# Kernel optimization log

Measured on AMD Instinct MI355X. Metric: run time of the kernel, lower is better.

The kernel has to match this reference:

```python
import jax, jax.numpy as jnp
import numpy as np

INPUT_SIZE = 512
HIDDEN_SIZE = 1024
BATCH = 16384


def setup_inputs() -> dict:
    key = jax.random.key(0)
    ks = jax.random.split(key, 11)
    s_x = 1.0 / np.sqrt(INPUT_SIZE)
    s_h = 1.0 / np.sqrt(HIDDEN_SIZE)
    inp = {
        "x": jax.random.normal(ks[0], (BATCH, INPUT_SIZE), dtype=jnp.float32),
        "hidden": jax.random.normal(ks[1], (BATCH, HIDDEN_SIZE), dtype=jnp.float32),
        # Linear weights stored as (in, out) for x @ W
        "Wxr": jax.random.uniform(ks[2], (INPUT_SIZE, HIDDEN_SIZE), jnp.float32, -s_x, s_x),
        "bxr": jax.random.uniform(ks[3], (HIDDEN_SIZE,), jnp.float32, -s_x, s_x),
        "Whr": jax.random.uniform(ks[4], (HIDDEN_SIZE, HIDDEN_SIZE), jnp.float32, -s_h, s_h),
        "Wxz": jax.random.uniform(ks[5], (INPUT_SIZE, HIDDEN_SIZE), jnp.float32, -s_x, s_x),
        "bxz": jax.random.uniform(ks[6], (HIDDEN_SIZE,), jnp.float32, -s_x, s_x),
        "Whz": jax.random.uniform(ks[7], (HIDDEN_SIZE, HIDDEN_SIZE), jnp.float32, -s_h, s_h),
        "Wxh": jax.random.uniform(ks[8], (INPUT_SIZE, HIDDEN_SIZE), jnp.float32, -s_x, s_x),
        "bxh": jax.random.uniform(ks[9], (HIDDEN_SIZE,), jnp.float32, -s_x, s_x),
        "Whh": jax.random.uniform(ks[10], (HIDDEN_SIZE, HIDDEN_SIZE), jnp.float32, -s_h, s_h),
    }
    return inp


def reference(x, hidden, Wxr, bxr, Whr, Wxz, bxz, Whz, Wxh, bxh, Whh):
    # GRU cell, single timestep.
    r = jax.nn.sigmoid(x @ Wxr + bxr + hidden @ Whr)          # reset gate (B,H)
    z = jax.nn.sigmoid(x @ Wxz + bxz + hidden @ Whz)          # update gate (B,H)
    h_cand = jnp.tanh(x @ Wxh + bxh + (r * hidden) @ Whh)     # candidate (B,H)
    return z * hidden + (1.0 - z) * h_cand
```

## Files before the change

kernel.cpp:

```cpp
#include <hip/hip_runtime.h>

typedef unsigned short u16;
typedef unsigned int u32;
typedef __bf16 bf16x8 __attribute__((ext_vector_type(8)));
typedef float f32x4 __attribute__((ext_vector_type(4)));

#define B_ROWS 16384
#define K1 1536

__device__ __forceinline__ u16 f2bf(float f) {
  u32 u = __float_as_uint(f);
  u = (u + 0x7fffu + ((u >> 16) & 1u)) >> 16;
  return (u16)u;
}
__device__ __forceinline__ float bf2f(u16 b) {
  return __uint_as_float(((u32)b) << 16);
}
__device__ __forceinline__ void gload_lds16(const void* g, void* l) {
  __builtin_amdgcn_global_load_lds((const __attribute__((address_space(1))) void*)g,
                                   (__attribute__((address_space(3))) void*)l,
                                   16, 0, 0);
}

__global__ void cvt_xh(const float* __restrict__ x, const float* __restrict__ h,
                       u16* __restrict__ xh) {
  const int iv = blockIdx.x * 256 + threadIdx.x;
  const int row = iv / 384;
  const int col = (iv - row * 384) * 4;
  const float* src = (col < 512) ? x + (size_t)row * 512 + col
                                 : h + (size_t)row * 1024 + (col - 512);
  float4 v = *(const float4*)src;
  u32 a = (u32)f2bf(v.x) | ((u32)f2bf(v.y) << 16);
  u32 b = (u32)f2bf(v.z) | ((u32)f2bf(v.w) << 16);
  *(uint2*)(xh + (size_t)row * 1536 + col) = make_uint2(a, b);
}

__global__ void transpose_cvt6(const float* __restrict__ Wxr, const float* __restrict__ Whr,
                               const float* __restrict__ Wxz, const float* __restrict__ Whz,
                               const float* __restrict__ Wxh, const float* __restrict__ Whh,
                               u16* __restrict__ W1t, u16* __restrict__ W2t) {
  __shared__ float tile[32][33];
  const int z = blockIdx.z;
  const float* W;
  u16* T;
  int Ks, koff, roff;
  switch (z) {
    case 0:  W = Wxr; T = W1t; Ks = 512;  koff = 0;   roff = 0;    break;
    case 1:  W = Whr; T = W1t; Ks = 1024; koff = 512; roff = 0;    break;
    case 2:  W = Wxz; T = W1t; Ks = 512;  koff = 0;   roff = 1024; break;
    case 3:  W = Whz; T = W1t; Ks = 1024; koff = 512; roff = 1024; break;
    case 4:  W = Wxh; T = W2t; Ks = 512;  koff = 0;   roff = 0;    break;
    default: W = Whh; T = W2t; Ks = 1024; koff = 512; roff = 0;    break;
  }
  const int bx = blockIdx.x, by = blockIdx.y;
  if (by * 32 >= Ks) return;
  const int tx = threadIdx.x, ty = threadIdx.y;
#pragma unroll
  for (int r = 0; r < 32; r += 8)
    tile[ty + r][tx] = W[(size_t)(by * 32 + ty + r) * 1024 + bx * 32 + tx];
  __syncthreads();
#pragma unroll
  for (int r = 0; r < 32; r += 8)
    T[(size_t)(roff + bx * 32 + ty + r) * K1 + koff + by * 32 + tx] = f2bf(tile[tx][ty + r]);
}

struct Src {
  const u16 *A, *B;
  u32 sA, sB;
};

__device__ __forceinline__ void gemm256(const Src& S, int nt, int brow, int bcol,
                                        u16* AsU, u16* BsU, f32x4 acc[8][4]) {
  const int tid = threadIdx.x;
  const int l = tid & 63;
  const int wid = tid >> 6;
  const int wr = wid >> 2, wc = wid & 3;
  const int lr = l & 15, kq = l >> 4;
  const int swzB = (lr & 7) * 16;
  const int kswzE = ((tid & 7) ^ ((tid >> 3) & 7)) * 8;
  const int r = tid >> 3;
  char* AsB = (char*)AsU;
  char* BsB = (char*)BsU;
  const int ldsQ = wid << 10;
  const int colK0 = (kq * 16) ^ swzB;
  const int colK1 = (64 + kq * 16) ^ swzB;
  int aRow[8], bRow[4];
#pragma unroll
  for (int m = 0; m < 8; ++m) aRow[m] = (wr * 128 + m * 16 + lr) * 128;
#pragma unroll
  for (int n = 0; n < 4; ++n) bRow[n] = (wc * 64 + n * 16 + lr) * 128;

  u32 offA[4], offB[4];
#pragma unroll
  for (int q = 0; q < 4; ++q) {
    offA[q] = (u32)((brow + q * 64 + r) * S.sA + kswzE) * 2u;
    offB[q] = (u32)((bcol + q * 64 + r) * S.sB + kswzE) * 2u;
  }

#define STG_A01(q_, c_) gload_lds16((const char*)S.A + offA[q_], \
    AsB + (c_) * 32768 + (q_) * 8192 + ldsQ)
#define STG_A23(q_, c_) gload_lds16((const char*)S.A + offA[q_], \
    AsB + (c_) * 32768 + 16384 + ((q_) - 2) * 8192 + ldsQ)
#define STG_B(q_, c_)   gload_lds16((const char*)S.B + offB[q_], \
    BsB + (c_) * 32768 + ((q_) >> 1) * 16384 + ((q_) & 1) * 8192 + ldsQ)

  STG_A01(0, 0); STG_A01(1, 0);
  STG_A23(2, 0); STG_A23(3, 0);
  STG_B(0, 0); STG_B(1, 0); STG_B(2, 0); STG_B(3, 0);
  offA[0] += 128; offA[1] += 128;
  STG_A01(0, 1); STG_A01(1, 1);
  offA[0] += 128; offA[1] += 128;
  offA[2] += 128; offA[3] += 128;
  offB[0] += 128; offB[1] += 128; offB[2] += 128; offB[3] += 128;
  asm volatile("s_waitcnt vmcnt(2)" ::: "memory");
  __builtin_amdgcn_s_barrier();
  asm volatile("" ::: "memory");

  for (int t = 0; t < nt; ++t) {
    const int c = t & 1;
    const int cb = c << 15;
    bf16x8 a[4][2], b[4][2];
#pragma unroll
    for (int m = 0; m < 4; ++m) {
      a[m][0] = *(const bf16x8*)(AsB + cb + aRow[m] + colK0);
      a[m][1] = *(const bf16x8*)(AsB + cb + aRow[m] + colK1);
    }
#pragma unroll
    for (int n = 0; n < 2; ++n) {
      b[n][0] = *(const bf16x8*)(BsB + cb + bRow[n] + colK0);
      b[n][1] = *(const bf16x8*)(BsB + cb + bRow[n] + colK1);
    }
    if (t + 1 < nt) { STG_A23(2, c ^ 1); STG_A23(3, c ^ 1); }
    __builtin_amdgcn_s_barrier();
    asm volatile("s_waitcnt lgkmcnt(0)" ::: "memory");
    __builtin_amdgcn_sched_barrier(0);
    __builtin_amdgcn_s_setprio(1);
#pragma unroll
    for (int kk = 0; kk < 2; ++kk)
#pragma unroll
      for (int m = 0; m < 4; ++m)
#pragma unroll
        for (int n = 0; n < 2; ++n)
          acc[m][n] = __builtin_amdgcn_mfma_f32_16x16x32_bf16(a[m][kk], b[n][kk], acc[m][n], 0, 0, 0);
    __builtin_amdgcn_s_setprio(0);
    __builtin_amdgcn_s_barrier();
    asm volatile("" ::: "memory");
#pragma unroll
    for (int n = 2; n < 4; ++n) {
      b[n][0] = *(const bf16x8*)(BsB + cb + bRow[n] + colK0);
      b[n][1] = *(const bf16x8*)(BsB + cb + bRow[n] + colK1);
    }
    if (t + 1 < nt) { STG_B(0, c ^ 1); STG_B(1, c ^ 1); }
    __builtin_amdgcn_s_barrier();
    asm volatile("s_waitcnt lgkmcnt(0)" ::: "memory");
    __builtin_amdgcn_sched_barrier(0);
    __builtin_amdgcn_s_setprio(1);
#pragma unroll
    for (int kk = 0; kk < 2; ++kk)
#pragma unroll
      for (int m = 0; m < 4; ++m)
#pragma unroll
        for (int n = 2; n < 4; ++n)
          acc[m][n] = __builtin_amdgcn_mfma_f32_16x16x32_bf16(a[m][kk], b[n][kk], acc[m][n], 0, 0, 0);
    __builtin_amdgcn_s_setprio(0);
    __builtin_amdgcn_s_barrier();
    asm volatile("" ::: "memory");
#pragma unroll
    for (int m = 0; m < 4; ++m) {
      a[m][0] = *(const bf16x8*)(AsB + cb + aRow[m + 4] + colK0);
      a[m][1] = *(const bf16x8*)(AsB + cb + aRow[m + 4] + colK1);
    }
    if (t + 1 < nt) { STG_B(2, c ^ 1); STG_B(3, c ^ 1); }
    __builtin_amdgcn_s_barrier();
    asm volatile("s_waitcnt lgkmcnt(0)" ::: "memory");
    __builtin_amdgcn_sched_barrier(0);
    __builtin_amdgcn_s_setprio(1);
#pragma unroll
    for (int kk = 0; kk < 2; ++kk)
#pragma unroll
      for (int m = 0; m < 4; ++m)
#pragma unroll
        for (int n = 2; n < 4; ++n)
          acc[m + 4][n] = __builtin_amdgcn_mfma_f32_16x16x32_bf16(a[m][kk], b[n][kk], acc[m + 4][n], 0, 0, 0);
    __builtin_amdgcn_s_setprio(0);
    __builtin_amdgcn_s_barrier();
    asm volatile("" ::: "memory");
    if (t + 2 < nt) { STG_A01(0, c); STG_A01(1, c); }
    __builtin_amdgcn_s_barrier();
    __builtin_amdgcn_s_setprio(1);
#pragma unroll
    for (int kk = 0; kk < 2; ++kk)
#pragma unroll
      for (int m = 0; m < 4; ++m)
#pragma unroll
        for (int n = 0; n < 2; ++n)
          acc[m + 4][n] = __builtin_amdgcn_mfma_f32_16x16x32_bf16(a[m][kk], b[n][kk], acc[m + 4][n], 0, 0, 0);
    __builtin_amdgcn_s_setprio(0);
    if (t + 2 < nt) { asm volatile("s_waitcnt vmcnt(2)" ::: "memory"); }
    else            { asm volatile("s_waitcnt vmcnt(0)" ::: "memory"); }
    __builtin_amdgcn_s_barrier();
    asm volatile("" ::: "memory");
    offA[0] += 128; offA[1] += 128; offA[2] += 128; offA[3] += 128;
    offB[0] += 128; offB[1] += 128; offB[2] += 128; offB[3] += 128;
  }
#undef STG_A01
#undef STG_A23
#undef STG_B
}

__global__ __launch_bounds__(512, 2) void gru_gemm1(
    const u16* __restrict__ xh, const u16* __restrict__ W1t,
    const float* __restrict__ bxr, const float* __restrict__ bxz,
    u16* __restrict__ rhb, u16* __restrict__ zb) {
  __shared__ __align__(16) u16 As[2 * 256 * 64];
  __shared__ __align__(16) u16 Bs[2 * 256 * 64];
  const int orig = blockIdx.x;
  const int slot = orig >> 3;
  const int mt = (orig & 7) + 8 * (slot >> 3);
  const int jt = slot & 7;
  const int brow = mt * 256;
  const int jcol = jt * 256;

  Src S { xh, W1t, K1, K1 };
  f32x4 acc[8][4] = {};
  gemm256(S, 24, brow, jcol, As, Bs, acc);

  const int l = threadIdx.x & 63;
  const int wid = threadIdx.x >> 6;
  const int wr = wid >> 2, wc = wid & 3;
  const int colb = jcol + wc * 64 + (l & 15);
  const int rowb = brow + wr * 128 + (l >> 4) * 4;
  if (jt < 4) {
#pragma unroll
    for (int n = 0; n < 4; ++n) {
      const int col = colb + n * 16;
      const float bias = bxr[col];
#pragma unroll
      for (int m = 0; m < 8; ++m)
#pragma unroll
        for (int j = 0; j < 4; ++j) {
          const int row = rowb + m * 16 + j;
          const float rg = 1.f / (1.f + __expf(-(acc[m][n][j] + bias)));
          const float hv = bf2f(xh[(size_t)row * K1 + 512 + col]);
          rhb[(size_t)row * 1024 + col] = f2bf(rg * hv);
        }
    }
  } else {
#pragma unroll
    for (int n = 0; n < 4; ++n) {
      const int col = colb + n * 16 - 1024;
      const float bias = bxz[col];
#pragma unroll
      for (int m = 0; m < 8; ++m)
#pragma unroll
        for (int j = 0; j < 4; ++j) {
          const int row = rowb + m * 16 + j;
          const float zg = 1.f / (1.f + __expf(-(acc[m][n][j] + bias)));
          zb[(size_t)row * 1024 + col] = f2bf(zg);
        }
    }
  }
}

__global__ __launch_bounds__(512, 2) void gru_gemm2(
    const u16* __restrict__ xh, const u16* __restrict__ rhb,
    const u16* __restrict__ W2t, const float* __restrict__ bxh,
    const u16* __restrict__ zb, float* __restrict__ out) {
  __shared__ __align__(16) u16 As[256 * 64];
  __shared__ __align__(16) u16 Bs[128 * 64];
  const int orig = blockIdx.x;
  const int wg = (orig & 7) * 64 + (orig >> 3);
  const int mt = wg & 63;
  const int jt = wg >> 6;
  const int brow = mt * 256;
  const int jcol = jt * 128;

  const int tid = threadIdx.x;
  const int l = tid & 63;
  const int wid = tid >> 6;
  const int wrk = wid >> 1, wc = wid & 1;
  const int lr = l & 15, kq = l >> 4;
  const int swzB = (lr & 7) * 16;
  const int kswzE = ((tid & 7) ^ ((tid >> 3) & 7)) * 8;
  const int r = tid >> 3;
  char* AsB = (char*)As;
  char* BsB = (char*)Bs;
  const int ldsQ = wid << 10;
  const int colK0 = (kq * 16) ^ swzB;
  const int colK1 = (64 + kq * 16) ^ swzB;
  int aRow[4], bRow[4];
#pragma unroll
  for (int m = 0; m < 4; ++m) aRow[m] = (wrk * 64 + m * 16 + lr) * 128;
#pragma unroll
  for (int n = 0; n < 4; ++n) bRow[n] = (wc * 64 + n * 16 + lr) * 128;

  const u16* pA = xh;
  u32 offA[4], offB[2];
#pragma unroll
  for (int q = 0; q < 4; ++q) offA[q] = (u32)((brow + q * 64 + r) * K1 + kswzE) * 2u;
#pragma unroll
  for (int q = 0; q < 2; ++q) offB[q] = (u32)((jcol + q * 64 + r) * K1 + kswzE) * 2u;

  f32x4 acc[4][4] = {};
  for (int t = 0; t < 24; ++t) {
    if (t == 8) {
      pA = rhb;
#pragma unroll
      for (int q = 0; q < 4; ++q) offA[q] = (u32)((brow + q * 64 + r) * 1024 + kswzE) * 2u;
    }
#pragma unroll
    for (int q = 0; q < 4; ++q)
      gload_lds16((const char*)pA + offA[q], AsB + q * 8192 + ldsQ);
#pragma unroll
    for (int q = 0; q < 2; ++q)
      gload_lds16((const char*)W2t + offB[q], BsB + q * 8192 + ldsQ);
    asm volatile("s_waitcnt vmcnt(0)" ::: "memory");
    __builtin_amdgcn_s_barrier();
    asm volatile("" ::: "memory");
    bf16x8 a[4][2], b[4][2];
#pragma unroll
    for (int n = 0; n < 4; ++n) {
      b[n][0] = *(const bf16x8*)(BsB + bRow[n] + colK0);
      b[n][1] = *(const bf16x8*)(BsB + bRow[n] + colK1);
    }
#pragma unroll
    for (int m = 0; m < 4; ++m) {
      a[m][0] = *(const bf16x8*)(AsB + aRow[m] + colK0);
      a[m][1] = *(const bf16x8*)(AsB + aRow[m] + colK1);
    }
    asm volatile("s_waitcnt lgkmcnt(0)" ::: "memory");
    __builtin_amdgcn_sched_barrier(0);
    __builtin_amdgcn_s_setprio(1);
#pragma unroll
    for (int kk = 0; kk < 2; ++kk)
#pragma unroll
      for (int m = 0; m < 4; ++m)
#pragma unroll
        for (int n = 0; n < 4; ++n)
          acc[m][n] = __builtin_amdgcn_mfma_f32_16x16x32_bf16(a[m][kk], b[n][kk], acc[m][n], 0, 0, 0);
    __builtin_amdgcn_s_setprio(0);
    __builtin_amdgcn_s_barrier();
    asm volatile("" ::: "memory");
#pragma unroll
    for (int q = 0; q < 4; ++q) offA[q] += 128;
#pragma unroll
    for (int q = 0; q < 2; ++q) offB[q] += 128;
  }

  const int colb = jcol + wc * 64 + (l & 15);
  const int rowb = brow + wrk * 64 + (l >> 4) * 4;
#pragma unroll
  for (int n = 0; n < 4; ++n) {
    const int col = colb + n * 16;
    const float bias = bxh[col];
#pragma unroll
    for (int m = 0; m < 4; ++m)
#pragma unroll
      for (int j = 0; j < 4; ++j) {
        const int row = rowb + m * 16 + j;
        const size_t idx = (size_t)row * 1024 + col;
        const float e = __expf(2.f * (acc[m][n][j] + bias));
        const float hc = 1.f - 2.f / (e + 1.f);
        const float z = bf2f(zb[idx]);
        const float h = bf2f(xh[(size_t)row * K1 + 512 + col]);
        out[idx] = z * h + (1.f - z) * hc;
      }
  }
}

extern "C" void kernel_launch(void* const* d_in, const int* in_sizes, int n_in,
                              void* d_out, int out_size, void* d_ws, size_t ws_size,
                              hipStream_t stream) {
  const float* x      = (const float*)d_in[0];
  const float* hidden = (const float*)d_in[1];
  const float* Wxr = (const float*)d_in[2];
  const float* bxr = (const float*)d_in[3];
  const float* Whr = (const float*)d_in[4];
  const float* Wxz = (const float*)d_in[5];
  const float* bxz = (const float*)d_in[6];
  const float* Whz = (const float*)d_in[7];
  const float* Wxh = (const float*)d_in[8];
  const float* bxh = (const float*)d_in[9];
  const float* Whh = (const float*)d_in[10];
  float* out = (float*)d_out;
  (void)in_sizes; (void)n_in; (void)out_size; (void)ws_size;

  char* p = (char*)d_ws;
  u16* xh  = (u16*)p; p += (size_t)B_ROWS * K1 * 2;
  u16* W1t = (u16*)p; p += (size_t)2048 * K1 * 2;
  u16* W2t = (u16*)p; p += (size_t)1024 * K1 * 2;
  u16* rhb = (u16*)p; p += (size_t)B_ROWS * 1024 * 2;
  u16* zb  = (u16*)p; p += (size_t)B_ROWS * 1024 * 2;

  cvt_xh<<<B_ROWS * 384 / 256, 256, 0, stream>>>(x, hidden, xh);
  transpose_cvt6<<<dim3(32, 32, 6), dim3(32, 8), 0, stream>>>(
      Wxr, Whr, Wxz, Whz, Wxh, Whh, W1t, W2t);

  gru_gemm1<<<512, 512, 0, stream>>>(xh, W1t, bxr, bxz, rhb, zb);
  gru_gemm2<<<512, 512, 0, stream>>>(xh, rhb, W2t, bxh, zb, out);
}
```

Before: 304.2 us.

## Double-buffer gemm2 LDS with interleaved quadrant prefetch; merge prep kernels

Restructures the second GEMM's K loop to double-buffer A and B tiles in LDS. Global-to-LDS loads for the next chunk are split into pieces and issued between four quadrant MFMA phases, so memory latency overlaps compute instead of waiting on vmcnt(0) every iteration. It also fuses the activation conversion and weight transpose kernels into one launch to save launch overhead. The trade-offs are doubled LDS use, which may limit occupancy under launch_bounds(512,2), more barriers per iteration, and delicate vmcnt accounting.

Measured after the change: 252.6 us. 17.0% less time.

```diff
diff --git a/kernel.cpp b/kernel.cpp
--- a/kernel.cpp
+++ b/kernel.cpp
@@ -22,25 +22,29 @@
                                    16, 0, 0);
 }
 
-__global__ void cvt_xh(const float* __restrict__ x, const float* __restrict__ h,
-                       u16* __restrict__ xh) {
-  const int iv = blockIdx.x * 256 + threadIdx.x;
-  const int row = iv / 384;
-  const int col = (iv - row * 384) * 4;
-  const float* src = (col < 512) ? x + (size_t)row * 512 + col
-                                 : h + (size_t)row * 1024 + (col - 512);
-  float4 v = *(const float4*)src;
-  u32 a = (u32)f2bf(v.x) | ((u32)f2bf(v.y) << 16);
-  u32 b = (u32)f2bf(v.z) | ((u32)f2bf(v.w) << 16);
-  *(uint2*)(xh + (size_t)row * 1536 + col) = make_uint2(a, b);
-}
-
-__global__ void transpose_cvt6(const float* __restrict__ Wxr, const float* __restrict__ Whr,
-                               const float* __restrict__ Wxz, const float* __restrict__ Whz,
-                               const float* __restrict__ Wxh, const float* __restrict__ Whh,
-                               u16* __restrict__ W1t, u16* __restrict__ W2t) {
+__global__ void prep(const float* __restrict__ x, const float* __restrict__ h,
+                     u16* __restrict__ xh,
+                     const float* __restrict__ Wxr, const float* __restrict__ Whr,
+                     const float* __restrict__ Wxz, const float* __restrict__ Whz,
+                     const float* __restrict__ Wxh, const float* __restrict__ Whh,
+                     u16* __restrict__ W1t, u16* __restrict__ W2t) {
+  if (blockIdx.x < 24576) {
+    const int iv = blockIdx.x * 256 + threadIdx.x;
+    const int row = iv / 384;
+    const int col = (iv - row * 384) * 4;
+    const float* src = (col < 512) ? x + (size_t)row * 512 + col
+                                   : h + (size_t)row * 1024 + (col - 512);
+    float4 v = *(const float4*)src;
+    u32 a = (u32)f2bf(v.x) | ((u32)f2bf(v.y) << 16);
+    u32 b = (u32)f2bf(v.z) | ((u32)f2bf(v.w) << 16);
+    *(uint2*)(xh + (size_t)row * 1536 + col) = make_uint2(a, b);
+    return;
+  }
   __shared__ float tile[32][33];
-  const int z = blockIdx.z;
+  const int idx2 = blockIdx.x - 24576;
+  const int z = idx2 >> 10;
+  const int rem = idx2 & 1023;
+  const int by = rem >> 5, bx = rem & 31;
   const float* W;
   u16* T;
   int Ks, koff, roff;
@@ -52,9 +56,8 @@
     case 4:  W = Wxh; T = W2t; Ks = 512;  koff = 0;   roff = 0;    break;
     default: W = Whh; T = W2t; Ks = 1024; koff = 512; roff = 0;    break;
   }
-  const int bx = blockIdx.x, by = blockIdx.y;
   if (by * 32 >= Ks) return;
-  const int tx = threadIdx.x, ty = threadIdx.y;
+  const int tx = threadIdx.x & 31, ty = threadIdx.x >> 5;
 #pragma unroll
   for (int r = 0; r < 32; r += 8)
     tile[ty + r][tx] = W[(size_t)(by * 32 + ty + r) * 1024 + bx * 32 + tx];
@@ -266,8 +269,8 @@
     const u16* __restrict__ xh, const u16* __restrict__ rhb,
     const u16* __restrict__ W2t, const float* __restrict__ bxh,
     const u16* __restrict__ zb, float* __restrict__ out) {
-  __shared__ __align__(16) u16 As[256 * 64];
-  __shared__ __align__(16) u16 Bs[128 * 64];
+  __shared__ __align__(16) u16 As[2 * 256 * 64];
+  __shared__ __align__(16) u16 Bs[2 * 128 * 64];
   const int orig = blockIdx.x;
   const int wg = (orig & 7) * 64 + (orig >> 3);
   const int mt = wg & 63;
@@ -294,58 +297,134 @@
 #pragma unroll
   for (int n = 0; n < 4; ++n) bRow[n] = (wc * 64 + n * 16 + lr) * 128;
 
-  const u16* pA = xh;
+  const u16* pA01 = xh;
+  const u16* pA23 = xh;
   u32 offA[4], offB[2];
 #pragma unroll
   for (int q = 0; q < 4; ++q) offA[q] = (u32)((brow + q * 64 + r) * K1 + kswzE) * 2u;
 #pragma unroll
   for (int q = 0; q < 2; ++q) offB[q] = (u32)((jcol + q * 64 + r) * K1 + kswzE) * 2u;
 
+#define G2_A01(q_, c_) gload_lds16((const char*)pA01 + offA[q_], \
+    AsB + (c_) * 32768 + (q_) * 8192 + ldsQ)
+#define G2_A23(q_, c_) gload_lds16((const char*)pA23 + offA[q_], \
+    AsB + (c_) * 32768 + 16384 + ((q_) - 2) * 8192 + ldsQ)
+#define G2_B(q_, c_)   gload_lds16((const char*)W2t + offB[q_], \
+    BsB + (c_) * 16384 + (q_) * 8192 + ldsQ)
+
+  G2_A01(0, 0); G2_A01(1, 0);
+  G2_A23(2, 0); G2_A23(3, 0);
+  G2_B(0, 0); G2_B(1, 0);
+  offA[0] += 128; offA[1] += 128;
+  G2_A01(0, 1); G2_A01(1, 1);
+  offA[0] += 128; offA[1] += 128;
+  offA[2] += 128; offA[3] += 128;
+  offB[0] += 128; offB[1] += 128;
+  asm volatile("s_waitcnt vmcnt(2)" ::: "memory");
+  __builtin_amdgcn_s_barrier();
+  asm volatile("" ::: "memory");
+
   f32x4 acc[4][4] = {};
-  for (int t = 0; t < 24; ++t) {
-    if (t == 8) {
-      pA = rhb;
-#pragma unroll
-      for (int q = 0; q < 4; ++q) offA[q] = (u32)((brow + q * 64 + r) * 1024 + kswzE) * 2u;
-    }
-#pragma unroll
-    for (int q = 0; q < 4; ++q)
-      gload_lds16((const char*)pA + offA[q], AsB + q * 8192 + ldsQ);
-#pragma unroll
-    for (int q = 0; q < 2; ++q)
-      gload_lds16((const char*)W2t + offB[q], BsB + q * 8192 + ldsQ);
-    asm volatile("s_waitcnt vmcnt(0)" ::: "memory");
-    __builtin_amdgcn_s_barrier();
-    asm volatile("" ::: "memory");
-    bf16x8 a[4][2], b[4][2];
-#pragma unroll
-    for (int n = 0; n < 4; ++n) {
-      b[n][0] = *(const bf16x8*)(BsB + bRow[n] + colK0);
-      b[n][1] = *(const bf16x8*)(BsB + bRow[n] + colK1);
-    }
-#pragma unroll
-    for (int m = 0; m < 4; ++m) {
-      a[m][0] = *(const bf16x8*)(AsB + aRow[m] + colK0);
-      a[m][1] = *(const bf16x8*)(AsB + aRow[m] + colK1);
-    }
-    asm volatile("s_waitcnt lgkmcnt(0)" ::: "memory");
-    __builtin_amdgcn_sched_barrier(0);
-    __builtin_amdgcn_s_setprio(1);
-#pragma unroll
-    for (int kk = 0; kk < 2; ++kk)
-#pragma unroll
-      for (int m = 0; m < 4; ++m)
-#pragma unroll
-        for (int n = 0; n < 4; ++n)
-          acc[m][n] = __builtin_amdgcn_mfma_f32_16x16x32_bf16(a[m][kk], b[n][kk], acc[m][n], 0, 0, 0);
-    __builtin_amdgcn_s_setprio(0);
-    __builtin_amdgcn_s_barrier();
-    asm volatile("" ::: "memory");
-#pragma unroll
-    for (int q = 0; q < 4; ++q) offA[q] += 128;
-#pragma unroll
-    for (int q = 0; q < 2; ++q) offB[q] += 128;
-  }
+  const int nt = 24;
+  for (int t = 0; t < nt; ++t) {
+    const int c = t & 1;
+    const int cbA = c << 15;
+    const int cbB = c << 14;
+    bf16x8 a01[2][2], a23[2][2], b01[2][2], b23[2][2];
+#pragma unroll
+    for (int m = 0; m < 2; ++m) {
+      a01[m][0] = *(const bf16x8*)(AsB + cbA + aRow[m] + colK0);
+      a01[m][1] = *(const bf16x8*)(AsB + cbA + aRow[m] + colK1);
+    }
+#pragma unroll
+    for (int n = 0; n < 2; ++n) {
+      b01[n][0] = *(const bf16x8*)(BsB + cbB + bRow[n] + colK0);
+      b01[n][1] = *(const bf16x8*)(BsB + cbB + bRow[n] + colK1);
+    }
+    if (t + 1 < nt) { G2_A23(2, c ^ 1); G2_A23(3, c ^ 1); }
+    __builtin_amdgcn_s_barrier();
+    asm volatile("s_waitcnt lgkmcnt(0)" ::: "memory");
+    __builtin_amdgcn_sched_barrier(0);
+    __builtin_amdgcn_s_setprio(1);
+#pragma unroll
+    for (int kk = 0; kk < 2; ++kk)
+#pragma unroll
+      for (int m = 0; m < 2; ++m)
+#pragma unroll
+        for (int n = 0; n < 2; ++n)
+          acc[m][n] = __builtin_amdgcn_mfma_f32_16x16x32_bf16(a01[m][kk], b01[n][kk], acc[m][n], 0, 0, 0);
+    __builtin_amdgcn_s_setprio(0);
+    __builtin_amdgcn_s_barrier();
+    asm volatile("" ::: "memory");
+#pragma unroll
+    for (int n = 0; n < 2; ++n) {
+      b23[n][0] = *(const bf16x8*)(BsB + cbB + bRow[n + 2] + colK0);
+      b23[n][1] = *(const bf16x8*)(BsB + cbB + bRow[n + 2] + colK1);
+    }
+    if (t + 1 < nt) { G2_B(0, c ^ 1); G2_B(1, c ^ 1); }
+    __builtin_amdgcn_s_barrier();
+    asm volatile("s_waitcnt lgkmcnt(0)" ::: "memory");
+    __builtin_amdgcn_sched_barrier(0);
+    __builtin_amdgcn_s_setprio(1);
+#pragma unroll
+    for (int kk = 0; kk < 2; ++kk)
+#pragma unroll
+      for (int m = 0; m < 2; ++m)
+#pragma unroll
+        for (int n = 0; n < 2; ++n)
+          acc[m][n + 2] = __builtin_amdgcn_mfma_f32_16x16x32_bf16(a01[m][kk], b23[n][kk], acc[m][n + 2], 0, 0, 0);
+    __builtin_amdgcn_s_setprio(0);
+    __builtin_amdgcn_s_barrier();
+    asm volatile("" ::: "memory");
+#pragma unroll
+    for (int m = 0; m < 2; ++m) {
+      a23[m][0] = *(const bf16x8*)(AsB + cbA + aRow[m + 2] + colK0);
+      a23[m][1] = *(const bf16x8*)(AsB + cbA + aRow[m + 2] + colK1);
+    }
+    __builtin_amdgcn_s_barrier();
+    asm volatile("s_waitcnt lgkmcnt(0)" ::: "memory");
+    __builtin_amdgcn_sched_barrier(0);
+    __builtin_amdgcn_s_setprio(1);
+#pragma unroll
+    for (int kk = 0; kk < 2; ++kk)
+#pragma unroll
+      for (int m = 0; m < 2; ++m)
+#pragma unroll
+        for (int n = 0; n < 2; ++n)
+          acc[m + 2][n + 2] = __builtin_amdgcn_mfma_f32_16x16x32_bf16(a23[m][kk], b23[n][kk], acc[m + 2][n + 2], 0, 0, 0);
+    __builtin_amdgcn_s_setprio(0);
+    __builtin_amdgcn_s_barrier();
+    asm volatile("" ::: "memory");
+    if (t + 2 < nt) { G2_A01(0, c); G2_A01(1, c); }
+    __builtin_amdgcn_s_barrier();
+    __builtin_amdgcn_s_setprio(1);
+#pragma unroll
+    for (int kk = 0; kk < 2; ++kk)
+#pragma unroll
+      for (int m = 0; m < 2; ++m)
+#pragma unroll
+        for (int n = 0; n < 2; ++n)
+          acc[m + 2][n] = __builtin_amdgcn_mfma_f32_16x16x32_bf16(a23[m][kk], b01[n][kk], acc[m + 2][n], 0, 0, 0);
+    __builtin_amdgcn_s_setprio(0);
+    if (t + 2 < nt) { asm volatile("s_waitcnt vmcnt(2)" ::: "memory"); }
+    else            { asm volatile("s_waitcnt vmcnt(0)" ::: "memory"); }
+    __builtin_amdgcn_s_barrier();
+    asm volatile("" ::: "memory");
+    if (t == 5) {
+      pA01 = rhb;
+      offA[0] = (u32)((brow + 0 * 64 + r) * 1024 + kswzE) * 2u;
+      offA[1] = (u32)((brow + 1 * 64 + r) * 1024 + kswzE) * 2u;
+    } else { offA[0] += 128; offA[1] += 128; }
+    if (t == 6) {
+      pA23 = rhb;
+      offA[2] = (u32)((brow + 2 * 64 + r) * 1024 + kswzE) * 2u;
+      offA[3] = (u32)((brow + 3 * 64 + r) * 1024 + kswzE) * 2u;
+    } else { offA[2] += 128; offA[3] += 128; }
+    offB[0] += 128; offB[1] += 128;
+  }
+#undef G2_A01
+#undef G2_A23
+#undef G2_B
 
   const int colb = jcol + wc * 64 + (l & 15);
   const int rowb = brow + wrk * 64 + (l >> 4) * 4;
@@ -392,10 +471,8 @@
   u16* rhb = (u16*)p; p += (size_t)B_ROWS * 1024 * 2;
   u16* zb  = (u16*)p; p += (size_t)B_ROWS * 1024 * 2;
 
-  cvt_xh<<<B_ROWS * 384 / 256, 256, 0, stream>>>(x, hidden, xh);
-  transpose_cvt6<<<dim3(32, 32, 6), dim3(32, 8), 0, stream>>>(
-      Wxr, Whr, Wxz, Whz, Wxh, Whh, W1t, W2t);
-
+  prep<<<24576 + 6144, 256, 0, stream>>>(x, hidden, xh,
+                                         Wxr, Whr, Wxz, Whz, Wxh, Whh, W1t, W2t);
   gru_gemm1<<<512, 512, 0, stream>>>(xh, W1t, bxr, bxz, rhb, zb);
   gru_gemm2<<<512, 512, 0, stream>>>(xh, rhb, W2t, bxh, zb, out);
 }
```
